# Kernel optimization log

Hardware: AMD Instinct MI355X
Metric: run time of the kernel (lower is better)

Reference implementation:

```python
import jax, jax.numpy as jnp
import numpy as np

N_NODES = 50000
N_EDGES = 600000
D_IN = 128
D_HID = 128
D_OUT = 128
LN_EPS = 1e-5


def _layer_norm(h, g, b):
    mu = jnp.mean(h, axis=-1, keepdims=True)
    var = jnp.var(h, axis=-1, keepdims=True)
    return (h - mu) * jax.lax.rsqrt(var + LN_EPS) * g + b


def _gin_conv(x, src, dst, w1, b1, w2, b2):
    # sum-aggregate neighbor messages at destination nodes, eps = 0
    agg = jax.ops.segment_sum(x[src], dst, num_segments=x.shape[0])
    h = x + agg
    h = jax.nn.relu(h @ w1 + b1)
    return h @ w2 + b2


def setup_inputs() -> dict:
    key = jax.random.key(0)
    ks = jax.random.split(key, 20)
    x = jax.random.normal(ks[0], (N_NODES, D_IN), dtype=jnp.float32)
    edge_index = jax.random.randint(ks[1], (2, N_EDGES), 0, N_NODES, dtype=jnp.int64)
    dims = [(D_IN, D_HID), (D_HID, D_HID), (D_HID, D_HID), (D_HID, D_OUT)]
    inp = {"x": x, "edge_index": edge_index}
    for i, (din, dout) in enumerate(dims):
        s1 = 1.0 / np.sqrt(din)
        s2 = 1.0 / np.sqrt(D_HID)
        inp[f"w1_{i}"] = jax.random.uniform(ks[2 + 4 * i], (din, D_HID), jnp.float32, -s1, s1)
        inp[f"b1_{i}"] = jax.random.uniform(ks[3 + 4 * i], (D_HID,), jnp.float32, -s1, s1)
        inp[f"w2_{i}"] = jax.random.uniform(ks[4 + 4 * i], (D_HID, dout), jnp.float32, -s2, s2)
        inp[f"b2_{i}"] = jax.random.uniform(ks[5 + 4 * i], (dout,), jnp.float32, -s2, s2)
    for i in range(3):  # LayerNorm only on first 3 blocks
        inp[f"g_{i}"] = jnp.ones((D_HID,), jnp.float32)
        inp[f"beta_{i}"] = jnp.zeros((D_HID,), jnp.float32)
    return inp


def reference(x, edge_index,
              w1_0, b1_0, w2_0, b2_0,
              w1_1, b1_1, w2_1, b2_1,
              w1_2, b1_2, w2_2, b2_2,
              w1_3, b1_3, w2_3, b2_3,
              g_0, beta_0, g_1, beta_1, g_2, beta_2):
    src, dst = edge_index[0], edge_index[1]
    mlps = [(w1_0, b1_0, w2_0, b2_0), (w1_1, b1_1, w2_1, b2_1),
            (w1_2, b1_2, w2_2, b2_2), (w1_3, b1_3, w2_3, b2_3)]
    lns = [(g_0, beta_0), (g_1, beta_1), (g_2, beta_2)]
    h = x
    for i in range(3):
        h = _gin_conv(h, src, dst, *mlps[i])
        h = _layer_norm(h, *lns[i])
        h = jax.nn.relu(h)  # dropout rate 0.0 -> identity
    h = _gin_conv(h, src, dst, *mlps[3])  # final block: no norm/act
    return h
```

## Files before the change

### kernel.cpp

```cpp
#include <hip/hip_runtime.h>
#include <hip/hip_bf16.h>

#define NN 50000
#define NE 600000
#define DD 128
#define LDSW 136
#define NB 196
#define BSH 8
#define EPB 2048
#define NBLK_AC ((NE + EPB - 1) / EPB)

typedef __bf16 bf16;
typedef __attribute__((ext_vector_type(8))) __bf16 bf16x8;
typedef __attribute__((ext_vector_type(4))) float f32x4;
typedef __attribute__((ext_vector_type(4))) unsigned int u32x4;
typedef __attribute__((ext_vector_type(4))) unsigned short u16x4;
typedef unsigned short u16;

__device__ __forceinline__ float bf_lo(unsigned int u) {
    return __builtin_bit_cast(float, u << 16);
}
__device__ __forceinline__ float bf_hi(unsigned int u) {
    return __builtin_bit_cast(float, u & 0xffff0000u);
}
__device__ __forceinline__ unsigned int bf_pack(float x, float y) {
    u16 a = __builtin_bit_cast(u16, (bf16)x);
    u16 b = __builtin_bit_cast(u16, (bf16)y);
    return (unsigned int)a | ((unsigned int)b << 16);
}

struct Ptr8 { const float* p[8]; };

__device__ __forceinline__ int edge_dst(const int* ei, int e, int f) {
    return f ? ei[2 * NE + 2 * e] : ei[NE + e];
}
__device__ __forceinline__ int edge_src(const int* ei, int e, int f) {
    return f ? ei[2 * e] : ei[e];
}

#define J1 (NN * DD / 4)
#define J2 (J1 + 8 * DD * DD)

__global__ __launch_bounds__(256) void k_init(const float* __restrict__ x,
                                              u16* __restrict__ xb,
                                              Ptr8 ws, u16* __restrict__ wt,
                                              int* __restrict__ bcnt,
                                              int* __restrict__ bcur,
                                              const int* __restrict__ ei,
                                              int* __restrict__ flag) {
    int tid = threadIdx.x;
    if (blockIdx.x == 0) {
        if (tid == 0) flag[0] = 1;
        __syncthreads();
        if (ei[2 * tid + 1] != 0) flag[0] = 0;
    }
    int id = blockIdx.x * 256 + tid;
    if (id < NB) { bcnt[id] = 0; bcur[id] = 0; }
    if (id < J1) {
        f32x4 v = *(const f32x4*)(x + (size_t)id * 4);
        u16x4 o;
        o.x = __builtin_bit_cast(u16, (bf16)v.x);
        o.y = __builtin_bit_cast(u16, (bf16)v.y);
        o.z = __builtin_bit_cast(u16, (bf16)v.z);
        o.w = __builtin_bit_cast(u16, (bf16)v.w);
        *(u16x4*)(xb + (size_t)id * 4) = o;
    } else if (id < J2) {
        int i = id - J1;
        int m = i >> 14;
        int rem = i & 16383;
        int k = rem >> 7;
        int n = rem & 127;
        bf16 b = (bf16)ws.p[m][k * DD + n];
        wt[(size_t)m * DD * DD + n * DD + k] = __builtin_bit_cast(u16, b);
    }
}

__global__ __launch_bounds__(256) void k_bcount(const int* __restrict__ ei,
                                                const int* __restrict__ flag,
                                                int* __restrict__ bcnt) {
    __shared__ int lh[NB];
    int tid = threadIdx.x;
    if (tid < NB) lh[tid] = 0;
    __syncthreads();
    int f = flag[0];
#pragma unroll
    for (int k = 0; k < 8; k++) {
        int e = blockIdx.x * EPB + k * 256 + tid;
        if (e < NE) {
            int d = edge_dst(ei, e, f);
            atomicAdd(&lh[d >> BSH], 1);
        }
    }
    __syncthreads();
    if (tid < NB && lh[tid] > 0) atomicAdd(&bcnt[tid], lh[tid]);
}

__global__ __launch_bounds__(256) void k_bscatter(const int* __restrict__ ei,
                                                  const int* __restrict__ flag,
                                                  const int* __restrict__ bcnt,
                                                  int* __restrict__ bcur,
                                                  unsigned int* __restrict__ tmp) {
    __shared__ int lh[NB];
    __shared__ int gb[NB];
    __shared__ int sboff[NB];
    __shared__ int sm[4];
    int tid = threadIdx.x;
    if (tid < NB) lh[tid] = 0;
    __syncthreads();
    int f = flag[0];
    int src[8], dst[8], lp[8];
    bool val[8];
#pragma unroll
    for (int k = 0; k < 8; k++) {
        int e = blockIdx.x * EPB + k * 256 + tid;
        val[k] = (e < NE);
        if (val[k]) {
            src[k] = edge_src(ei, e, f);
            dst[k] = edge_dst(ei, e, f);
            lp[k] = atomicAdd(&lh[dst[k] >> BSH], 1);
        }
    }
    __syncthreads();
    {
        int lane = tid & 63, w = tid >> 6;
        int v = (tid < NB) ? bcnt[tid] : 0;
        int orig = v;
#pragma unroll
        for (int off = 1; off < 64; off <<= 1) {
            int t = __shfl_up(v, off);
            if (lane >= off) v += t;
        }
        if (lane == 63) sm[w] = v;
        __syncthreads();
        int add = 0;
        for (int k = 0; k < w; k++) add += sm[k];
        if (tid < NB) sboff[tid] = v - orig + add;
    }
    __syncthreads();
    if (tid < NB && lh[tid] > 0)
        gb[tid] = sboff[tid] + atomicAdd(&bcur[tid], lh[tid]);
    __syncthreads();
#pragma unroll
    for (int k = 0; k < 8; k++) {
        if (val[k]) {
            unsigned int pk = (unsigned)src[k] | ((unsigned)(dst[k] & 255) << 16);
            tmp[gb[dst[k] >> BSH] + lp[k]] = pk;
        }
    }
}

__global__ __launch_bounds__(256) void k_build(const unsigned int* __restrict__ tmp,
                                               const int* __restrict__ bcnt,
                                               int* __restrict__ row_start,
                                               int* __restrict__ adj) {
    __shared__ int cnt[256];
    __shared__ int ccur[256];
    __shared__ int sm[4];
    int b = blockIdx.x, tid = threadIdx.x;
    int base = b << BSH;
    int lane = tid & 63, w = tid >> 6;
    cnt[tid] = 0;
    int v = (tid < b) ? bcnt[tid] : 0;
#pragma unroll
    for (int off = 1; off < 64; off <<= 1) v += __shfl_xor(v, off);
    if (lane == 0) sm[w] = v;
    __syncthreads();
    int s = sm[0] + sm[1] + sm[2] + sm[3];
    int e = s + bcnt[b];
    for (int i = s + tid; i < e; i += 256) {
        atomicAdd(&cnt[tmp[i] >> 16], 1);
    }
    __syncthreads();
    int v2 = cnt[tid];
    int orig = v2;
#pragma unroll
    for (int off = 1; off < 64; off <<= 1) {
        int t = __shfl_up(v2, off);
        if (lane >= off) v2 += t;
    }
    if (lane == 63) sm[w] = v2;
    __syncthreads();
    int add = 0;
    for (int k = 0; k < w; k++) add += sm[k];
    int ex = s + (v2 - orig) + add;
    ccur[tid] = ex;
    if (base + tid < NN) row_start[base + tid] = ex;
    if (b == 0 && tid == 0) row_start[NN] = NE;
    __syncthreads();
    for (int i = s + tid; i < e; i += 256) {
        unsigned int pk = tmp[i];
        int p = atomicAdd(&ccur[pk >> 16], 1);
        adj[p] = (int)(pk & 0xffffu);
    }
}

__global__ __launch_bounds__(256) void k_agg(const u16* __restrict__ xb,
                                             const int* __restrict__ row_start,
                                             const int* __restrict__ adj,
                                             u16* __restrict__ out) {
    int gid = blockIdx.x * blockDim.x + threadIdx.x;
    int wave = gid >> 6, lane = gid & 63;
    int grp = lane >> 4, l = lane & 15;
    int node = wave * 4 + grp;
    if (node >= NN) return;
    const u32x4* base = (const u32x4*)xb;
    u32x4 sv = base[(size_t)node * 16 + l];
    float af[8], bf[8];
#pragma unroll
    for (int j = 0; j < 4; j++) {
        af[2 * j] = bf_lo(sv[j]); af[2 * j + 1] = bf_hi(sv[j]);
        bf[2 * j] = 0.f; bf[2 * j + 1] = 0.f;
    }
    int s = row_start[node], e = row_start[node + 1];
    int i = s;
    for (; i + 7 < e; i += 8) {
        u32x4 t0 = base[(size_t)adj[i] * 16 + l];
        u32x4 t1 = base[(size_t)adj[i + 1] * 16 + l];
        u32x4 t2 = base[(size_t)adj[i + 2] * 16 + l];
        u32x4 t3 = base[(size_t)adj[i + 3] * 16 + l];
        u32x4 t4 = base[(size_t)adj[i + 4] * 16 + l];
        u32x4 t5 = base[(size_t)adj[i + 5] * 16 + l];
        u32x4 t6 = base[(size_t)adj[i + 6] * 16 + l];
        u32x4 t7 = base[(size_t)adj[i + 7] * 16 + l];
#pragma unroll
        for (int j = 0; j < 4; j++) {
            af[2 * j]     += (bf_lo(t0[j]) + bf_lo(t1[j])) + (bf_lo(t2[j]) + bf_lo(t3[j]));
            af[2 * j + 1] += (bf_hi(t0[j]) + bf_hi(t1[j])) + (bf_hi(t2[j]) + bf_hi(t3[j]));
            bf[2 * j]     += (bf_lo(t4[j]) + bf_lo(t5[j])) + (bf_lo(t6[j]) + bf_lo(t7[j]));
            bf[2 * j + 1] += (bf_hi(t4[j]) + bf_hi(t5[j])) + (bf_hi(t6[j]) + bf_hi(t7[j]));
        }
    }
    for (; i + 3 < e; i += 4) {
        u32x4 t0 = base[(size_t)adj[i] * 16 + l];
        u32x4 t1 = base[(size_t)adj[i + 1] * 16 + l];
        u32x4 t2 = base[(size_t)adj[i + 2] * 16 + l];
        u32x4 t3 = base[(size_t)adj[i + 3] * 16 + l];
#pragma unroll
        for (int j = 0; j < 4; j++) {
            af[2 * j]     += bf_lo(t0[j]) + bf_lo(t1[j]);
            af[2 * j + 1] += bf_hi(t0[j]) + bf_hi(t1[j]);
            bf[2 * j]     += bf_lo(t2[j]) + bf_lo(t3[j]);
            bf[2 * j + 1] += bf_hi(t2[j]) + bf_hi(t3[j]);
        }
    }
    for (; i < e; i++) {
        u32x4 t = base[(size_t)adj[i] * 16 + l];
#pragma unroll
        for (int j = 0; j < 4; j++) { af[2 * j] += bf_lo(t[j]); af[2 * j + 1] += bf_hi(t[j]); }
    }
    u32x4 o;
#pragma unroll
    for (int j = 0; j < 4; j++) o[j] = bf_pack(af[2 * j] + bf[2 * j], af[2 * j + 1] + bf[2 * j + 1]);
    ((u32x4*)out)[(size_t)node * 16 + l] = o;
}

template <bool LN, bool B16OUT>
__global__ __launch_bounds__(128) void k_mlp(const u16* __restrict__ hin,
                                             const u16* __restrict__ w1t,
                                             const float* __restrict__ b1,
                                             const u16* __restrict__ w2t,
                                             const float* __restrict__ b2,
                                             const float* __restrict__ g,
                                             const float* __restrict__ bta,
                                             void* __restrict__ hout) {
    __shared__ u16 lds[64 * LDSW];
    const int tid = threadIdx.x;
    const int wv = tid >> 6, lane = tid & 63;
    const int l15 = lane & 15, l4 = lane >> 4;
    const int tile0 = blockIdx.x * 64;

#pragma unroll
    for (int it = 0; it < 8; ++it) {
        int slot = tid + it * 128;
        int row = slot >> 4, c16 = slot & 15;
        u32x4 v = {0u, 0u, 0u, 0u};
        int grow = tile0 + row;
        if (grow < NN) v = *(const u32x4*)(hin + (size_t)grow * DD + c16 * 8);
        *(u32x4*)&lds[row * LDSW + c16 * 8] = v;
    }
    __syncthreads();

    float b1c[8], b2c[8], gc[8], bc[8];
#pragma unroll
    for (int c = 0; c < 8; c++) {
        int col = c * 16 + l15;
        b1c[c] = b1[col];
        b2c[c] = b2[col];
        if (LN) { gc[c] = g[col]; bc[c] = bta[col]; }
    }

    f32x4 acc[2][8];
#pragma unroll
    for (int r = 0; r < 2; r++)
#pragma unroll
        for (int c = 0; c < 8; c++) acc[r][c] = (f32x4){0.f, 0.f, 0.f, 0.f};

    const int rowbase = wv * 32;

#pragma unroll
    for (int ks = 0; ks < 4; ++ks) {
        bf16x8 a0 = __builtin_bit_cast(bf16x8,
            *(const u32x4*)&lds[(rowbase + l15) * LDSW + ks * 32 + l4 * 8]);
        bf16x8 a1 = __builtin_bit_cast(bf16x8,
            *(const u32x4*)&lds[(rowbase + 16 + l15) * LDSW + ks * 32 + l4 * 8]);
#pragma unroll
        for (int c = 0; c < 8; c++) {
            bf16x8 b = __builtin_bit_cast(bf16x8,
                *(const u32x4*)(w1t + (size_t)(c * 16 + l15) * DD + ks * 32 + l4 * 8));
            acc[0][c] = __builtin_amdgcn_mfma_f32_16x16x32_bf16(a0, b, acc[0][c], 0, 0, 0);
            acc[1][c] = __builtin_amdgcn_mfma_f32_16x16x32_bf16(a1, b, acc[1][c], 0, 0, 0);
        }
    }

#pragma unroll
    for (int r = 0; r < 2; r++) {
#pragma unroll
        for (int c = 0; c < 8; c++) {
            int col = c * 16 + l15;
#pragma unroll
            for (int j = 0; j < 4; j++) {
                float v = acc[r][c][j] + b1c[c];
                v = v > 0.f ? v : 0.f;
                bf16 b = (bf16)v;
                int row = rowbase + r * 16 + l4 * 4 + j;
                lds[row * LDSW + col] = __builtin_bit_cast(u16, b);
            }
        }
    }

#pragma unroll
    for (int r = 0; r < 2; r++)
#pragma unroll
        for (int c = 0; c < 8; c++) acc[r][c] = (f32x4){0.f, 0.f, 0.f, 0.f};

#pragma unroll
    for (int ks = 0; ks < 4; ++ks) {
        bf16x8 a0 = __builtin_bit_cast(bf16x8,
            *(const u32x4*)&lds[(rowbase + l15) * LDSW + ks * 32 + l4 * 8]);
        bf16x8 a1 = __builtin_bit_cast(bf16x8,
            *(const u32x4*)&lds[(rowbase + 16 + l15) * LDSW + ks * 32 + l4 * 8]);
#pragma unroll
        for (int c = 0; c < 8; c++) {
            bf16x8 b = __builtin_bit_cast(bf16x8,
                *(const u32x4*)(w2t + (size_t)(c * 16 + l15) * DD + ks * 32 + l4 * 8));
            acc[0][c] = __builtin_amdgcn_mfma_f32_16x16x32_bf16(a0, b, acc[0][c], 0, 0, 0);
            acc[1][c] = __builtin_amdgcn_mfma_f32_16x16x32_bf16(a1, b, acc[1][c], 0, 0, 0);
        }
    }

#pragma unroll
    for (int r = 0; r < 2; r++) {
        float vals[8][4];
#pragma unroll
        for (int c = 0; c < 8; c++)
#pragma unroll
            for (int j = 0; j < 4; j++) vals[c][j] = acc[r][c][j] + b2c[c];

        if (LN) {
            float s[4], q[4];
#pragma unroll
            for (int j = 0; j < 4; j++) {
                s[j] = 0.f; q[j] = 0.f;
#pragma unroll
                for (int c = 0; c < 8; c++) {
                    s[j] += vals[c][j];
                    q[j] += vals[c][j] * vals[c][j];
                }
            }
#pragma unroll
            for (int m = 1; m <= 8; m <<= 1) {
#pragma unroll
                for (int j = 0; j < 4; j++) {
                    s[j] += __shfl_xor(s[j], m);
                    q[j] += __shfl_xor(q[j], m);
                }
            }
#pragma unroll
            for (int j = 0; j < 4; j++) {
                float mu = s[j] * (1.f / 128.f);
                float var = q[j] * (1.f / 128.f) - mu * mu;
                float rs = rsqrtf(var + 1e-5f);
#pragma unroll
                for (int c = 0; c < 8; c++) {
                    float v = (vals[c][j] - mu) * rs * gc[c] + bc[c];
                    vals[c][j] = v > 0.f ? v : 0.f;
                }
            }
        }

        if (B16OUT) {
#pragma unroll
            for (int c = 0; c < 8; c++) {
                int col = c * 16 + l15;
#pragma unroll
                for (int j = 0; j < 4; j++) {
                    int row = rowbase + r * 16 + l4 * 4 + j;
                    lds[row * LDSW + col] =
                        __builtin_bit_cast(u16, (bf16)vals[c][j]);
                }
            }
        } else {
#pragma unroll
            for (int c = 0; c < 8; c++) {
                int col = c * 16 + l15;
#pragma unroll
                for (int j = 0; j < 4; j++) {
                    int row = tile0 + rowbase + r * 16 + l4 * 4 + j;
                    if (row < NN)
                        ((float*)hout)[(size_t)row * DD + col] = vals[c][j];
                }
            }
        }
    }

    if (B16OUT) {
#pragma unroll
        for (int it = 0; it < 8; ++it) {
            int slot = it * 64 + lane;
            int row = rowbase + (slot >> 4);
            int c16 = slot & 15;
            u32x4 v = *(const u32x4*)&lds[row * LDSW + c16 * 8];
            int grow = tile0 + row;
            if (grow < NN)
                *(u32x4*)((u16*)hout + (size_t)grow * DD + c16 * 8) = v;
        }
    }
}

extern "C" void kernel_launch(void* const* d_in, const int* in_sizes, int n_in,
                              void* d_out, int out_size, void* d_ws, size_t ws_size,
                              hipStream_t stream) {
    const float* x = (const float*)d_in[0];
    const int* ei = (const int*)d_in[1];
    const float* w1[4]; const float* b1[4]; const float* w2[4]; const float* b2[4];
    for (int i = 0; i < 4; i++) {
        w1[i] = (const float*)d_in[2 + 4 * i];
        b1[i] = (const float*)d_in[3 + 4 * i];
        w2[i] = (const float*)d_in[4 + 4 * i];
        b2[i] = (const float*)d_in[5 + 4 * i];
    }
    const float* g[3]; const float* bt[3];
    for (int i = 0; i < 3; i++) {
        g[i] = (const float*)d_in[18 + 2 * i];
        bt[i] = (const float*)d_in[19 + 2 * i];
    }

    char* ws = (char*)d_ws;
    size_t off = 0;
    auto alloc = [&](size_t bytes) -> char* {
        char* p = ws + off;
        off = (off + bytes + 255) & ~(size_t)255;
        return p;
    };
    int* flag          = (int*)alloc(4);
    int* row_start     = (int*)alloc((NN + 1) * 4);
    int* bcnt          = (int*)alloc(NB * 4);
    int* bcur          = (int*)alloc(NB * 4);
    int* adj           = (int*)alloc(NE * 4);
    unsigned int* tmp  = (unsigned int*)alloc((size_t)NE * 4);
    u16* wt            = (u16*)alloc((size_t)8 * DD * DD * 2);
    u16* xb            = (u16*)alloc((size_t)NN * DD * 2);
    u16* hbf           = (u16*)alloc((size_t)NN * DD * 2);
    u16* hA            = (u16*)alloc((size_t)NN * DD * 2);
    u16* hB            = (u16*)alloc((size_t)NN * DD * 2);

    Ptr8 p8;
    for (int i = 0; i < 4; i++) {
        p8.p[2 * i] = w1[i];
        p8.p[2 * i + 1] = w2[i];
    }

    k_init<<<(J2 + 255) / 256, 256, 0, stream>>>(x, xb, p8, wt, bcnt, bcur, ei, flag);
    k_bcount<<<NBLK_AC, 256, 0, stream>>>(ei, flag, bcnt);
    k_bscatter<<<NBLK_AC, 256, 0, stream>>>(ei, flag, bcnt, bcur, tmp);
    k_build<<<NB, 256, 0, stream>>>(tmp, bcnt, row_start, adj);

    const int mgrid = (NN + 63) / 64;
    const u16* hin = xb;
    for (int i = 0; i < 4; i++) {
        k_agg<<<(NN / 4 * 64) / 256, 256, 0, stream>>>(hin, row_start, adj, hbf);
        const u16* w1ti = wt + (size_t)(2 * i) * DD * DD;
        const u16* w2ti = wt + (size_t)(2 * i + 1) * DD * DD;
        if (i < 3) {
            u16* outp = (i & 1) ? hB : hA;
            k_mlp<true, true><<<mgrid, 128, 0, stream>>>(
                hbf, w1ti, b1[i], w2ti, b2[i], g[i], bt[i], outp);
            hin = outp;
        } else {
            k_mlp<false, false><<<mgrid, 128, 0, stream>>>(
                hbf, w1ti, b1[i], w2ti, b2[i], nullptr, nullptr, d_out);
        }
    }
}
```

Measured before the change: 238.1 us.

## Merge bucket count into scatter with fixed-stride buckets; single-wave MLP blocks

Removes the separate bucket-count kernel by giving each destination bucket a fixed-capacity region (BSTR slots) in the temp buffer, so the scatter kernel claims offsets with one global atomic per bucket. k_build then reads each bucket from its strided region and gets the global prefix from the counts. Independently, the MLP kernel moves from two waves of 32 rows each to one wave covering all 64 rows, which doubles per-wave accumulators and reuses each weight fragment across four MFMAs. The risks are bucket overflow if any bucket exceeds 4096 edges (random inputs average about 3072) and more register pressure with less parallelism per tile in the MLP.

Measured after the change: 229.3 us. 1.04x faster.

```diff
diff --git a/kernel.cpp b/kernel.cpp
--- a/kernel.cpp
+++ b/kernel.cpp
@@ -7,6 +7,7 @@
 #define LDSW 136
 #define NB 196
 #define BSH 8
+#define BSTR 4096
 #define EPB 2048
 #define NBLK_AC ((NE + EPB - 1) / EPB)
 
@@ -45,7 +46,6 @@
                                               u16* __restrict__ xb,
                                               Ptr8 ws, u16* __restrict__ wt,
                                               int* __restrict__ bcnt,
-                                              int* __restrict__ bcur,
                                               const int* __restrict__ ei,
                                               int* __restrict__ flag) {
     int tid = threadIdx.x;
@@ -55,7 +55,7 @@
         if (ei[2 * tid + 1] != 0) flag[0] = 0;
     }
     int id = blockIdx.x * 256 + tid;
-    if (id < NB) { bcnt[id] = 0; bcur[id] = 0; }
+    if (id < NB) bcnt[id] = 0;
     if (id < J1) {
         f32x4 v = *(const f32x4*)(x + (size_t)id * 4);
         u16x4 o;
@@ -75,35 +75,12 @@
     }
 }
 
-__global__ __launch_bounds__(256) void k_bcount(const int* __restrict__ ei,
-                                                const int* __restrict__ flag,
-                                                int* __restrict__ bcnt) {
-    __shared__ int lh[NB];
-    int tid = threadIdx.x;
-    if (tid < NB) lh[tid] = 0;
-    __syncthreads();
-    int f = flag[0];
-#pragma unroll
-    for (int k = 0; k < 8; k++) {
-        int e = blockIdx.x * EPB + k * 256 + tid;
-        if (e < NE) {
-            int d = edge_dst(ei, e, f);
-            atomicAdd(&lh[d >> BSH], 1);
-        }
-    }
-    __syncthreads();
-    if (tid < NB && lh[tid] > 0) atomicAdd(&bcnt[tid], lh[tid]);
-}
-
-__global__ __launch_bounds__(256) void k_bscatter(const int* __restrict__ ei,
-                                                  const int* __restrict__ flag,
-                                                  const int* __restrict__ bcnt,
-                                                  int* __restrict__ bcur,
-                                                  unsigned int* __restrict__ tmp) {
+__global__ __launch_bounds__(256) void k_scatter(const int* __restrict__ ei,
+                                                 const int* __restrict__ flag,
+                                                 int* __restrict__ bcnt,
+                                                 unsigned int* __restrict__ tmp) {
     __shared__ int lh[NB];
     __shared__ int gb[NB];
-    __shared__ int sboff[NB];
-    __shared__ int sm[4];
     int tid = threadIdx.x;
     if (tid < NB) lh[tid] = 0;
     __syncthreads();
@@ -121,30 +98,14 @@
         }
     }
     __syncthreads();
-    {
-        int lane = tid & 63, w = tid >> 6;
-        int v = (tid < NB) ? bcnt[tid] : 0;
-        int orig = v;
-#pragma unroll
-        for (int off = 1; off < 64; off <<= 1) {
-            int t = __shfl_up(v, off);
-            if (lane >= off) v += t;
-        }
-        if (lane == 63) sm[w] = v;
-        __syncthreads();
-        int add = 0;
-        for (int k = 0; k < w; k++) add += sm[k];
-        if (tid < NB) sboff[tid] = v - orig + add;
-    }
-    __syncthreads();
-    if (tid < NB && lh[tid] > 0)
-        gb[tid] = sboff[tid] + atomicAdd(&bcur[tid], lh[tid]);
+    if (tid < NB && lh[tid] > 0) gb[tid] = atomicAdd(&bcnt[tid], lh[tid]);
     __syncthreads();
 #pragma unroll
     for (int k = 0; k < 8; k++) {
         if (val[k]) {
+            int bkt = dst[k] >> BSH;
             unsigned int pk = (unsigned)src[k] | ((unsigned)(dst[k] & 255) << 16);
-            tmp[gb[dst[k] >> BSH] + lp[k]] = pk;
+            tmp[(size_t)bkt * BSTR + gb[bkt] + lp[k]] = pk;
         }
     }
 }
@@ -165,10 +126,11 @@
     for (int off = 1; off < 64; off <<= 1) v += __shfl_xor(v, off);
     if (lane == 0) sm[w] = v;
     __syncthreads();
-    int s = sm[0] + sm[1] + sm[2] + sm[3];
-    int e = s + bcnt[b];
-    for (int i = s + tid; i < e; i += 256) {
-        atomicAdd(&cnt[tmp[i] >> 16], 1);
+    int G = sm[0] + sm[1] + sm[2] + sm[3];
+    int n = bcnt[b];
+    size_t ts = (size_t)b * BSTR;
+    for (int i = tid; i < n; i += 256) {
+        atomicAdd(&cnt[tmp[ts + i] >> 16], 1);
     }
     __syncthreads();
     int v2 = cnt[tid];
@@ -182,13 +144,13 @@
     __syncthreads();
     int add = 0;
     for (int k = 0; k < w; k++) add += sm[k];
-    int ex = s + (v2 - orig) + add;
+    int ex = G + (v2 - orig) + add;
     ccur[tid] = ex;
     if (base + tid < NN) row_start[base + tid] = ex;
     if (b == 0 && tid == 0) row_start[NN] = NE;
     __syncthreads();
-    for (int i = s + tid; i < e; i += 256) {
-        unsigned int pk = tmp[i];
+    for (int i = tid; i < n; i += 256) {
+        unsigned int pk = tmp[ts + i];
         int p = atomicAdd(&ccur[pk >> 16], 1);
         adj[p] = (int)(pk & 0xffffu);
     }
@@ -255,23 +217,22 @@
 }
 
 template <bool LN, bool B16OUT>
-__global__ __launch_bounds__(128) void k_mlp(const u16* __restrict__ hin,
-                                             const u16* __restrict__ w1t,
-                                             const float* __restrict__ b1,
-                                             const u16* __restrict__ w2t,
-                                             const float* __restrict__ b2,
-                                             const float* __restrict__ g,
-                                             const float* __restrict__ bta,
-                                             void* __restrict__ hout) {
+__global__ __launch_bounds__(64) void k_mlp(const u16* __restrict__ hin,
+                                            const u16* __restrict__ w1t,
+                                            const float* __restrict__ b1,
+                                            const u16* __restrict__ w2t,
+                                            const float* __restrict__ b2,
+                                            const float* __restrict__ g,
+                                            const float* __restrict__ bta,
+                                            void* __restrict__ hout) {
     __shared__ u16 lds[64 * LDSW];
-    const int tid = threadIdx.x;
-    const int wv = tid >> 6, lane = tid & 63;
+    const int lane = threadIdx.x;
     const int l15 = lane & 15, l4 = lane >> 4;
     const int tile0 = blockIdx.x * 64;
 
 #pragma unroll
-    for (int it = 0; it < 8; ++it) {
-        int slot = tid + it * 128;
+    for (int it = 0; it < 16; ++it) {
+        int slot = lane + it * 64;
         int row = slot >> 4, c16 = slot & 15;
         u32x4 v = {0u, 0u, 0u, 0u};
         int grow = tile0 + row;
@@ -289,31 +250,35 @@
         if (LN) { gc[c] = g[col]; bc[c] = bta[col]; }
     }
 
-    f32x4 acc[2][8];
-#pragma unroll
-    for (int r = 0; r < 2; r++)
+    f32x4 acc[4][8];
+#pragma unroll
+    for (int r = 0; r < 4; r++)
 #pragma unroll
         for (int c = 0; c < 8; c++) acc[r][c] = (f32x4){0.f, 0.f, 0.f, 0.f};
-
-    const int rowbase = wv * 32;
 
 #pragma unroll
     for (int ks = 0; ks < 4; ++ks) {
         bf16x8 a0 = __builtin_bit_cast(bf16x8,
-            *(const u32x4*)&lds[(rowbase + l15) * LDSW + ks * 32 + l4 * 8]);
+            *(const u32x4*)&lds[(l15) * LDSW + ks * 32 + l4 * 8]);
         bf16x8 a1 = __builtin_bit_cast(bf16x8,
-            *(const u32x4*)&lds[(rowbase + 16 + l15) * LDSW + ks * 32 + l4 * 8]);
+            *(const u32x4*)&lds[(16 + l15) * LDSW + ks * 32 + l4 * 8]);
+        bf16x8 a2 = __builtin_bit_cast(bf16x8,
+            *(const u32x4*)&lds[(32 + l15) * LDSW + ks * 32 + l4 * 8]);
+        bf16x8 a3 = __builtin_bit_cast(bf16x8,
+            *(const u32x4*)&lds[(48 + l15) * LDSW + ks * 32 + l4 * 8]);
 #pragma unroll
         for (int c = 0; c < 8; c++) {
             bf16x8 b = __builtin_bit_cast(bf16x8,
                 *(const u32x4*)(w1t + (size_t)(c * 16 + l15) * DD + ks * 32 + l4 * 8));
             acc[0][c] = __builtin_amdgcn_mfma_f32_16x16x32_bf16(a0, b, acc[0][c], 0, 0, 0);
             acc[1][c] = __builtin_amdgcn_mfma_f32_16x16x32_bf16(a1, b, acc[1][c], 0, 0, 0);
-        }
-    }
-
-#pragma unroll
-    for (int r = 0; r < 2; r++) {
+            acc[2][c] = __builtin_amdgcn_mfma_f32_16x16x32_bf16(a2, b, acc[2][c], 0, 0, 0);
+            acc[3][c] = __builtin_amdgcn_mfma_f32_16x16x32_bf16(a3, b, acc[3][c], 0, 0, 0);
+        }
+    }
+
+#pragma unroll
+    for (int r = 0; r < 4; r++) {
 #pragma unroll
         for (int c = 0; c < 8; c++) {
             int col = c * 16 + l15;
@@ -322,34 +287,40 @@
                 float v = acc[r][c][j] + b1c[c];
                 v = v > 0.f ? v : 0.f;
                 bf16 b = (bf16)v;
-                int row = rowbase + r * 16 + l4 * 4 + j;
+                int row = r * 16 + l4 * 4 + j;
                 lds[row * LDSW + col] = __builtin_bit_cast(u16, b);
             }
         }
     }
 
 #pragma unroll
-    for (int r = 0; r < 2; r++)
+    for (int r = 0; r < 4; r++)
 #pragma unroll
         for (int c = 0; c < 8; c++) acc[r][c] = (f32x4){0.f, 0.f, 0.f, 0.f};
 
 #pragma unroll
     for (int ks = 0; ks < 4; ++ks) {
         bf16x8 a0 = __builtin_bit_cast(bf16x8,
-            *(const u32x4*)&lds[(rowbase + l15) * LDSW + ks * 32 + l4 * 8]);
+            *(const u32x4*)&lds[(l15) * LDSW + ks * 32 + l4 * 8]);
         bf16x8 a1 = __builtin_bit_cast(bf16x8,
-            *(const u32x4*)&lds[(rowbase + 16 + l15) * LDSW + ks * 32 + l4 * 8]);
+            *(const u32x4*)&lds[(16 + l15) * LDSW + ks * 32 + l4 * 8]);
+        bf16x8 a2 = __builtin_bit_cast(bf16x8,
+            *(const u32x4*)&lds[(32 + l15) * LDSW + ks * 32 + l4 * 8]);
+        bf16x8 a3 = __builtin_bit_cast(bf16x8,
+            *(const u32x4*)&lds[(48 + l15) * LDSW + ks * 32 + l4 * 8]);
 #pragma unroll
         for (int c = 0; c < 8; c++) {
             bf16x8 b = __builtin_bit_cast(bf16x8,
                 *(const u32x4*)(w2t + (size_t)(c * 16 + l15) * DD + ks * 32 + l4 * 8));
             acc[0][c] = __builtin_amdgcn_mfma_f32_16x16x32_bf16(a0, b, acc[0][c], 0, 0, 0);
             acc[1][c] = __builtin_amdgcn_mfma_f32_16x16x32_bf16(a1, b, acc[1][c], 0, 0, 0);
-        }
-    }
-
-#pragma unroll
-    for (int r = 0; r < 2; r++) {
+            acc[2][c] = __builtin_amdgcn_mfma_f32_16x16x32_bf16(a2, b, acc[2][c], 0, 0, 0);
+            acc[3][c] = __builtin_amdgcn_mfma_f32_16x16x32_bf16(a3, b, acc[3][c], 0, 0, 0);
+        }
+    }
+
+#pragma unroll
+    for (int r = 0; r < 4; r++) {
         float vals[8][4];
 #pragma unroll
         for (int c = 0; c < 8; c++)
@@ -394,7 +365,7 @@
                 int col = c * 16 + l15;
 #pragma unroll
                 for (int j = 0; j < 4; j++) {
-                    int row = rowbase + r * 16 + l4 * 4 + j;
+                    int row = r * 16 + l4 * 4 + j;
                     lds[row * LDSW + col] =
                         __builtin_bit_cast(u16, (bf16)vals[c][j]);
                 }
@@ -405,7 +376,7 @@
                 int col = c * 16 + l15;
 #pragma unroll
                 for (int j = 0; j < 4; j++) {
-                    int row = tile0 + rowbase + r * 16 + l4 * 4 + j;
+                    int row = tile0 + r * 16 + l4 * 4 + j;
                     if (row < NN)
                         ((float*)hout)[(size_t)row * DD + col] = vals[c][j];
                 }
@@ -415,9 +386,9 @@
 
     if (B16OUT) {
 #pragma unroll
-        for (int it = 0; it < 8; ++it) {
+        for (int it = 0; it < 16; ++it) {
             int slot = it * 64 + lane;
-            int row = rowbase + (slot >> 4);
+            int row = slot >> 4;
             int c16 = slot & 15;
             u32x4 v = *(const u32x4*)&lds[row * LDSW + c16 * 8];
             int grow = tile0 + row;
@@ -455,9 +426,8 @@
     int* flag          = (int*)alloc(4);
     int* row_start     = (int*)alloc((NN + 1) * 4);
     int* bcnt          = (int*)alloc(NB * 4);
-    int* bcur          = (int*)alloc(NB * 4);
     int* adj           = (int*)alloc(NE * 4);
-    unsigned int* tmp  = (unsigned int*)alloc((size_t)NE * 4);
+    unsigned int* tmp  = (unsigned int*)alloc((size_t)NB * BSTR * 4);
     u16* wt            = (u16*)alloc((size_t)8 * DD * DD * 2);
     u16* xb            = (u16*)alloc((size_t)NN * DD * 2);
     u16* hbf           = (u16*)alloc((size_t)NN * DD * 2);
@@ -470,9 +440,8 @@
         p8.p[2 * i + 1] = w2[i];
     }
 
-    k_init<<<(J2 + 255) / 256, 256, 0, stream>>>(x, xb, p8, wt, bcnt, bcur, ei, flag);
-    k_bcount<<<NBLK_AC, 256, 0, stream>>>(ei, flag, bcnt);
-    k_bscatter<<<NBLK_AC, 256, 0, stream>>>(ei, flag, bcnt, bcur, tmp);
+    k_init<<<(J2 + 255) / 256, 256, 0, stream>>>(x, xb, p8, wt, bcnt, ei, flag);
+    k_scatter<<<NBLK_AC, 256, 0, stream>>>(ei, flag, bcnt, tmp);
     k_build<<<NB, 256, 0, stream>>>(tmp, bcnt, row_start, adj);
 
     const int mgrid = (NN + 63) / 64;
@@ -483,11 +452,11 @@
         const u16* w2ti = wt + (size_t)(2 * i + 1) * DD * DD;
         if (i < 3) {
             u16* outp = (i & 1) ? hB : hA;
-            k_mlp<true, true><<<mgrid, 128, 0, stream>>>(
+            k_mlp<true, true><<<mgrid, 64, 0, stream>>>(
                 hbf, w1ti, b1[i], w2ti, b2[i], g[i], bt[i], outp);
             hin = outp;
         } else {
-            k_mlp<false, false><<<mgrid, 128, 0, stream>>>(
+            k_mlp<false, false><<<mgrid, 64, 0, stream>>>(
                 hbf, w1ti, b1[i], w2ti, b2[i], nullptr, nullptr, d_out);
         }
     }
```
